# Kernel optimization log

Measured on AMD Instinct MI355X. Metric: run time of the kernel, lower is better.

## Reference

```python
import jax, jax.numpy as jnp
import numpy as np

N_HEAD = 16
NEG = -1e9

def setup_inputs() -> dict:
    key = jax.random.key(0)
    ks = jax.random.split(key, 11)
    B, T, D = 2, 2048, 1024
    s = 0.02
    return {
        "x": jax.random.normal(ks[0], (B, T, D), jnp.float32),
        "mask": jax.random.randint(ks[1], (B, T), 0, 2).astype(bool),
        "wq": jax.random.normal(ks[2], (D, D), jnp.float32) * s,
        "bq": jax.random.normal(ks[3], (D,), jnp.float32) * s,
        "wk": jax.random.normal(ks[4], (D, D), jnp.float32) * s,
        "bk": jax.random.normal(ks[5], (D,), jnp.float32) * s,
        "wv": jax.random.normal(ks[6], (D, D), jnp.float32) * s,
        "bv": jax.random.normal(ks[7], (D,), jnp.float32) * s,
        "wp": jax.random.normal(ks[8], (D, D), jnp.float32) * s,
        "bp": jax.random.normal(ks[9], (D,), jnp.float32) * s,
    }

def reference(x, mask, wq, bq, wk, bk, wv, bv, wp, bp):
    B, T, V = x.shape
    H = N_HEAD
    hd = V // H
    # project and split heads: [B, H, T, hd]
    def heads(w, b):
        return (x @ w + b).reshape(B, T, H, hd).transpose(0, 2, 1, 3)
    q = heads(wq, bq)
    k = heads(wk, bk)
    v = heads(wv, bv)
    # scores [B, H, T, T]
    att = jnp.einsum("bhqd,bhkd->bhqk", q, k) * (1.0 / jnp.sqrt(jnp.float32(hd)))
    # key-padding mask: True -> masked. broadcast [B,1,1,T] == torch's [B,1,T,T]
    att = jnp.where(mask[:, None, None, :], NEG, att)
    att = jax.nn.softmax(att, axis=-1)
    out = jnp.einsum("bhqk,bhkd->bhqd", att, v)  # [B,H,T,hd]
    out = out.transpose(0, 2, 1, 3).reshape(B, T, V)
    out = out @ wp + bp
    # dropout is identity in eval mode
    return out, att
```

## Files before the change

kernel.cpp:

```cpp
#include <hip/hip_runtime.h>
#include <stdint.h>
#include <stddef.h>


typedef __attribute__((ext_vector_type(8))) short short8;
typedef __attribute__((ext_vector_type(4))) float f32x4;

#define LDS_AS __attribute__((address_space(3)))
#define GLB_AS __attribute__((address_space(1)))

static __device__ __forceinline__ unsigned short f2bf(float f) {
  union { float f; uint32_t u; } v; v.f = f;
  uint32_t u = v.u;
  return (unsigned short)((u + 0x7fffu + ((u >> 16) & 1u)) >> 16);
}

static __device__ __forceinline__ void gload16(const void* g, void* l) {
  __builtin_amdgcn_global_load_lds((const GLB_AS uint32_t*)g, (LDS_AS uint32_t*)l, 16, 0, 0);
}

static __device__ __forceinline__ f32x4 mfma16(short8 a, short8 b, f32x4 c) {
  return __builtin_amdgcn_mfma_f32_16x16x32_bf16(a, b, c, 0, 0, 0);
}

__global__ void k_convert_x(const float* __restrict__ x, unsigned short* __restrict__ xb) {
  int i = blockIdx.x * 256 + threadIdx.x;
  float4 v = ((const float4*)x)[i];
  ushort4 o;
  o.x = f2bf(v.x); o.y = f2bf(v.y); o.z = f2bf(v.z); o.w = f2bf(v.w);
  ((ushort4*)xb)[i] = o;
}

__global__ void k_mask(const int* __restrict__ m, float* __restrict__ madd) {
  int i = blockIdx.x * 256 + threadIdx.x;
  madd[i] = m[i] ? -1e9f : 0.0f;
}

__global__ void k_transpose_w(const float* __restrict__ w0, const float* __restrict__ w1,
                              const float* __restrict__ w2, const float* __restrict__ w3,
                              unsigned short* __restrict__ o0, unsigned short* __restrict__ o1,
                              unsigned short* __restrict__ o2, unsigned short* __restrict__ o3) {
  int bx = blockIdx.x;
  int which = bx >> 8, tile = bx & 255;
  const float* w = which == 0 ? w0 : which == 1 ? w1 : which == 2 ? w2 : w3;
  unsigned short* o = which == 0 ? o0 : which == 1 ? o1 : which == 2 ? o2 : o3;
  int k0 = (tile >> 4) << 6, n0 = (tile & 15) << 6;
  __shared__ float t[64][65];
  int tid = threadIdx.x;
  int r = tid >> 4, c4 = (tid & 15) << 2;
#pragma unroll
  for (int i = 0; i < 4; i++) {
    int row = r + (i << 4);
    float4 v = *(const float4*)(w + (size_t)(k0 + row) * 1024 + n0 + c4);
    t[row][c4] = v.x; t[row][c4 + 1] = v.y; t[row][c4 + 2] = v.z; t[row][c4 + 3] = v.w;
  }
  __syncthreads();
#pragma unroll
  for (int i = 0; i < 4; i++) {
    int n = r + (i << 4);
    ushort4 ov;
    ov.x = f2bf(t[c4 + 0][n]); ov.y = f2bf(t[c4 + 1][n]);
    ov.z = f2bf(t[c4 + 2][n]); ov.w = f2bf(t[c4 + 3][n]);
    *(ushort4*)(o + (size_t)(n0 + n) * 1024 + k0 + c4) = ov;
  }
}

static __device__ __forceinline__ void gemm_tile(const unsigned short* __restrict__ A,
                                                 const unsigned short* __restrict__ Bt,
                                                 int m0, int n0,
                                                 f32x4 acc[4][4], char* ldsA, char* ldsB) {
  const int tid = threadIdx.x;
  const int l = tid & 63;
  const int wr = tid >> 7;
  const int wc = (tid >> 6) & 1;
  const int arow0 = wr * 64 + (l & 15);
  const int brow0 = wc * 64 + (l & 15);
  const int srow = tid >> 3;
  const int sgi = tid & 7;

  for (int kt = 0; kt < 1024; kt += 64) {
    __syncthreads();
#pragma unroll
    for (int c = 0; c < 4; c++) {
      int row = c * 32 + srow;
      int soff = (sgi ^ (row & 7)) << 3;
      gload16(A + (size_t)(m0 + row) * 1024 + kt + soff, ldsA + (c * 256 + tid) * 16);
      gload16(Bt + (size_t)(n0 + row) * 1024 + kt + soff, ldsB + (c * 256 + tid) * 16);
    }
    asm volatile("s_waitcnt vmcnt(0)" ::: "memory");
    __syncthreads();
#pragma unroll
    for (int ks = 0; ks < 2; ks++) {
      const int kbyte = ks * 64 + ((l >> 4) << 4);
      short8 a[4], b[4];
#pragma unroll
      for (int i = 0; i < 4; i++) {
        int row = arow0 + i * 16;
        a[i] = *(const short8*)(ldsA + row * 128 + (kbyte ^ ((row & 7) << 4)));
      }
#pragma unroll
      for (int j = 0; j < 4; j++) {
        int row = brow0 + j * 16;
        b[j] = *(const short8*)(ldsB + row * 128 + (kbyte ^ ((row & 7) << 4)));
      }
#pragma unroll
      for (int i = 0; i < 4; i++)
#pragma unroll
        for (int j = 0; j < 4; j++)
          acc[i][j] = mfma16(a[i], b[j], acc[i][j]);
    }
  }
}

__global__ __launch_bounds__(256) void k_gemm_qkv(const unsigned short* __restrict__ xb,
    const unsigned short* __restrict__ wqt, const unsigned short* __restrict__ wkt,
    const unsigned short* __restrict__ wvt,
    const float* __restrict__ bq, const float* __restrict__ bk, const float* __restrict__ bv,
    unsigned short* __restrict__ Q, unsigned short* __restrict__ K, unsigned short* __restrict__ Vt) {
  __shared__ __align__(16) char smem[32768];
  char* ldsA = smem;
  char* ldsB = smem + 16384;
  const int mat = blockIdx.y >> 3;
  const int nb = blockIdx.y & 7;
  const unsigned short* Bt = mat == 0 ? wqt : mat == 1 ? wkt : wvt;
  const float* bias = mat == 0 ? bq : mat == 1 ? bk : bv;
  const int m0 = blockIdx.x * 128, n0 = nb * 128;

  f32x4 acc[4][4] = {};
  gemm_tile(xb, Bt, m0, n0, acc, ldsA, ldsB);

  const int tid = threadIdx.x, l = tid & 63;
  const int wr = tid >> 7, wc = (tid >> 6) & 1;
  if (mat < 2) {
    unsigned short* O = (mat == 0) ? Q : K;
#pragma unroll
    for (int j = 0; j < 4; j++) {
      int col = n0 + wc * 64 + j * 16 + (l & 15);
      float bv_ = bias[col];
      int h = col >> 6, d = col & 63;
#pragma unroll
      for (int i = 0; i < 4; i++) {
        int row0 = m0 + wr * 64 + i * 16 + ((l >> 4) << 2);
#pragma unroll
        for (int e = 0; e < 4; e++) {
          int row = row0 + e;
          int b = row >> 11, t = row & 2047;
          O[(((size_t)(b * 16 + h)) * 2048 + t) * 64 + d] = f2bf(acc[i][j][e] + bv_);
        }
      }
    }
  } else {
#pragma unroll
    for (int j = 0; j < 4; j++) {
      int col = n0 + wc * 64 + j * 16 + (l & 15);
      float bv_ = bias[col];
      int h = col >> 6, d = col & 63;
#pragma unroll
      for (int i = 0; i < 4; i++) {
        int row0 = m0 + wr * 64 + i * 16 + ((l >> 4) << 2);
        int b = row0 >> 11, t0 = row0 & 2047;
        ushort4 pk;
        pk.x = f2bf(acc[i][j][0] + bv_);
        pk.y = f2bf(acc[i][j][1] + bv_);
        pk.z = f2bf(acc[i][j][2] + bv_);
        pk.w = f2bf(acc[i][j][3] + bv_);
        *(ushort4*)(Vt + ((size_t)(b * 16 + h) * 64 + d) * 2048 + t0) = pk;
      }
    }
  }
}

__global__ __launch_bounds__(256) void k_gemm_proj(const unsigned short* __restrict__ ctx,
    const unsigned short* __restrict__ wpt, const float* __restrict__ bp,
    float* __restrict__ out) {
  __shared__ __align__(16) char smem[32768];
  char* ldsA = smem;
  char* ldsB = smem + 16384;
  const int m0 = blockIdx.x * 128, n0 = blockIdx.y * 128;
  f32x4 acc[4][4] = {};
  gemm_tile(ctx, wpt, m0, n0, acc, ldsA, ldsB);
  const int tid = threadIdx.x, l = tid & 63;
  const int wr = tid >> 7, wc = (tid >> 6) & 1;
#pragma unroll
  for (int j = 0; j < 4; j++) {
    int col = n0 + wc * 64 + j * 16 + (l & 15);
    float bv_ = bp[col];
#pragma unroll
    for (int i = 0; i < 4; i++) {
      int row0 = m0 + wr * 64 + i * 16 + ((l >> 4) << 2);
#pragma unroll
      for (int e = 0; e < 4; e++)
        out[(size_t)(row0 + e) * 1024 + col] = acc[i][j][e] + bv_;
    }
  }
}

__global__ __launch_bounds__(256) void k_attn(const unsigned short* __restrict__ Q,
    const unsigned short* __restrict__ K, const unsigned short* __restrict__ Vt,
    const float* __restrict__ maskadd, float* __restrict__ att,
    unsigned short* __restrict__ ctx) {
  __shared__ __align__(16) char smem[57344];
  char* Ql = smem;
  char* Kl = smem + 8192;
  char* Vl = smem + 24576;
  char* Pl = smem + 40960;

  const int bid = (blockIdx.x & 7) * 128 + (blockIdx.x >> 3);
  const int qb = bid & 31, bh = bid >> 5;
  const int b = bh >> 4, h = bh & 15;
  const int tid = threadIdx.x, w = tid >> 6, l = tid & 63;
  const int qbase = qb * 64;

  const unsigned short* Qg = Q + (size_t)bh * 2048 * 64;
  const unsigned short* Kg = K + (size_t)bh * 2048 * 64;
  const unsigned short* Vg = Vt + (size_t)bh * 64 * 2048;
  const float* mg = maskadd + b * 2048;
  const float scale = 0.125f;

#pragma unroll
  for (int c = 0; c < 2; c++) {
    int g = c * 256 + tid;
    int row = g >> 3, gi = tid & 7;
    gload16(Qg + (size_t)(qbase + row) * 64 + ((gi ^ (row & 7)) << 3), Ql + g * 16);
  }
  asm volatile("s_waitcnt vmcnt(0)" ::: "memory");
  __syncthreads();

  short8 qf[2];
  {
    int row = w * 16 + (l & 15);
#pragma unroll
    for (int ks = 0; ks < 2; ks++) {
      int kbyte = ks * 64 + ((l >> 4) << 4);
      qf[ks] = *(const short8*)(Ql + row * 128 + (kbyte ^ ((row & 7) << 4)));
    }
  }

  float mrow[4], srow[4];
#pragma unroll
  for (int e = 0; e < 4; e++) { mrow[e] = -1e30f; srow[e] = 0.0f; }

  for (int ch = 0; ch < 16; ch++) {
    __syncthreads();
#pragma unroll
    for (int c = 0; c < 4; c++) {
      int g = c * 256 + tid;
      int row = g >> 3, gi = tid & 7;
      gload16(Kg + (size_t)(ch * 128 + row) * 64 + ((gi ^ (row & 7)) << 3), Kl + g * 16);
    }
    asm volatile("s_waitcnt vmcnt(0)" ::: "memory");
    __syncthreads();

    float lv[8][4];
    float cmax[4] = {-1e30f, -1e30f, -1e30f, -1e30f};
#pragma unroll
    for (int nt = 0; nt < 8; nt++) {
      f32x4 s = {};
#pragma unroll
      for (int ks = 0; ks < 2; ks++) {
        int row = nt * 16 + (l & 15);
        int kbyte = ks * 64 + ((l >> 4) << 4);
        short8 kf = *(const short8*)(Kl + row * 128 + (kbyte ^ ((row & 7) << 4)));
        s = mfma16(qf[ks], kf, s);
      }
      int key = ch * 128 + nt * 16 + (l & 15);
      float madd = mg[key];
#pragma unroll
      for (int e = 0; e < 4; e++) {
        lv[nt][e] = s[e] * scale + madd;
        cmax[e] = fmaxf(cmax[e], lv[nt][e]);
      }
    }
#pragma unroll
    for (int e = 0; e < 4; e++) {
      float cs = 0.0f;
#pragma unroll
      for (int nt = 0; nt < 8; nt++) cs += __expf(lv[nt][e] - cmax[e]);
      float mn = fmaxf(mrow[e], cmax[e]);
      srow[e] = srow[e] * __expf(mrow[e] - mn) + cs * __expf(cmax[e] - mn);
      mrow[e] = mn;
    }
  }

  float invs[4];
#pragma unroll
  for (int e = 0; e < 4; e++) {
    float m = mrow[e], s = srow[e];
#pragma unroll
    for (int msk = 1; msk < 16; msk <<= 1) {
      float mo = __shfl_xor(m, msk);
      float so = __shfl_xor(s, msk);
      float mn = fmaxf(m, mo);
      s = s * __expf(m - mn) + so * __expf(mo - mn);
      m = mn;
    }
    mrow[e] = m;
    invs[e] = 1.0f / s;
  }

  f32x4 o[4] = {};
  for (int ch = 0; ch < 16; ch++) {
    __syncthreads();
#pragma unroll
    for (int c = 0; c < 4; c++) {
      int g = c * 256 + tid;
      int row = g >> 3, gi = tid & 7;
      gload16(Kg + (size_t)(ch * 128 + row) * 64 + ((gi ^ (row & 7)) << 3), Kl + g * 16);
    }
#pragma unroll
    for (int c = 0; c < 4; c++) {
      int g = c * 256 + tid;
      int d = g >> 4, gi = tid & 15;
      gload16(Vg + (size_t)d * 2048 + ch * 128 + ((gi ^ (d & 7)) << 3), Vl + g * 16);
    }
    asm volatile("s_waitcnt vmcnt(0)" ::: "memory");
    __syncthreads();

#pragma unroll
    for (int nt = 0; nt < 8; nt++) {
      f32x4 s = {};
#pragma unroll
      for (int ks = 0; ks < 2; ks++) {
        int row = nt * 16 + (l & 15);
        int kbyte = ks * 64 + ((l >> 4) << 4);
        short8 kf = *(const short8*)(Kl + row * 128 + (kbyte ^ ((row & 7) << 4)));
        s = mfma16(qf[ks], kf, s);
      }
      int key = ch * 128 + nt * 16 + (l & 15);
      float madd = mg[key];
#pragma unroll
      for (int e = 0; e < 4; e++) {
        float p = __expf(s[e] * scale + madd - mrow[e]) * invs[e];
        int qrow = qbase + w * 16 + ((l >> 4) << 2) + e;
        __builtin_nontemporal_store(p, att + ((size_t)bh * 2048 + qrow) * 2048 + key);
        int pr = w * 16 + ((l >> 4) << 2) + e;
        int cb = (nt * 16 + (l & 15)) * 2;
        *(unsigned short*)(Pl + pr * 256 + (cb ^ ((pr & 7) << 4))) = f2bf(p);
      }
    }
#pragma unroll
    for (int ks = 0; ks < 4; ks++) {
      int prow = w * 16 + (l & 15);
      int kb = ks * 64 + ((l >> 4) << 4);
      short8 pa = *(const short8*)(Pl + prow * 256 + (kb ^ ((prow & 7) << 4)));
#pragma unroll
      for (int dt = 0; dt < 4; dt++) {
        int vrow = dt * 16 + (l & 15);
        short8 vb = *(const short8*)(Vl + vrow * 256 + (kb ^ ((vrow & 7) << 4)));
        o[dt] = mfma16(pa, vb, o[dt]);
      }
    }
  }

#pragma unroll
  for (int dt = 0; dt < 4; dt++) {
#pragma unroll
    for (int e = 0; e < 4; e++) {
      int t = qbase + w * 16 + ((l >> 4) << 2) + e;
      int col = h * 64 + dt * 16 + (l & 15);
      ctx[((size_t)(b * 2048 + t)) * 1024 + col] = f2bf(o[dt][e]);
    }
  }
}

extern "C" void kernel_launch(void* const* d_in, const int* in_sizes, int n_in,
                              void* d_out, int out_size, void* d_ws, size_t ws_size,
                              hipStream_t stream) {
  const float* x  = (const float*)d_in[0];
  const int* mask = (const int*)d_in[1];
  const float* wq = (const float*)d_in[2];
  const float* bq = (const float*)d_in[3];
  const float* wk = (const float*)d_in[4];
  const float* bk = (const float*)d_in[5];
  const float* wv = (const float*)d_in[6];
  const float* bv = (const float*)d_in[7];
  const float* wp = (const float*)d_in[8];
  const float* bp = (const float*)d_in[9];

  float* out = (float*)d_out;
  float* att = out + 4194304;

  char* ws = (char*)d_ws;
  unsigned short* xb  = (unsigned short*)(ws);
  unsigned short* wqt = (unsigned short*)(ws + 8388608);
  unsigned short* wkt = (unsigned short*)(ws + 10485760);
  unsigned short* wvt = (unsigned short*)(ws + 12582912);
  unsigned short* wpt = (unsigned short*)(ws + 14680064);
  unsigned short* Qw  = (unsigned short*)(ws + 16777216);
  unsigned short* Kw  = (unsigned short*)(ws + 25165824);
  unsigned short* Vtw = (unsigned short*)(ws + 33554432);
  unsigned short* ctx = (unsigned short*)(ws + 41943040);
  float* madd         = (float*)(ws + 50331648);

  k_convert_x<<<4096, 256, 0, stream>>>(x, xb);
  k_mask<<<16, 256, 0, stream>>>(mask, madd);
  k_transpose_w<<<1024, 256, 0, stream>>>(wq, wk, wv, wp, wqt, wkt, wvt, wpt);
  k_gemm_qkv<<<dim3(32, 24), 256, 0, stream>>>(xb, wqt, wkt, wvt, bq, bk, bv, Qw, Kw, Vtw);
  k_attn<<<1024, 256, 0, stream>>>(Qw, Kw, Vtw, madd, att, ctx);
  k_gemm_proj<<<dim3(32, 8), 256, 0, stream>>>(ctx, wpt, bp, out);
}
```

Baseline: 266.3 us.

## Process 128 query rows per attention block to halve K/V reloads

Each attention block now handles 128 query rows instead of 64. Each wave owns two 16-row sub-tiles, so every K and V tile loaded into LDS is reused across twice as many queries, and the grid shrinks from 1024 to 512 blocks. The P buffer is aliased onto the Q staging area, with an extra barrier after Q fragments are read, and LDS grows to 64KB. The trade-off is higher register pressure, fewer blocks per CU and fewer total blocks, which may reduce occupancy and latency hiding. The kernel is likely bound by the fp32 attention-matrix write, so the K/V savings may matter little.

```diff
diff --git a/kernel.cpp b/kernel.cpp
--- a/kernel.cpp
+++ b/kernel.cpp
@@ -199,17 +199,17 @@
     const unsigned short* __restrict__ K, const unsigned short* __restrict__ Vt,
     const float* __restrict__ maskadd, float* __restrict__ att,
     unsigned short* __restrict__ ctx) {
-  __shared__ __align__(16) char smem[57344];
+  __shared__ __align__(16) char smem[65536];
+  char* Pl = smem;
   char* Ql = smem;
-  char* Kl = smem + 8192;
-  char* Vl = smem + 24576;
-  char* Pl = smem + 40960;
-
-  const int bid = (blockIdx.x & 7) * 128 + (blockIdx.x >> 3);
-  const int qb = bid & 31, bh = bid >> 5;
+  char* Kl = smem + 32768;
+  char* Vl = smem + 49152;
+
+  const int bid = (blockIdx.x & 7) * 64 + (blockIdx.x >> 3);
+  const int qb = bid & 15, bh = bid >> 4;
   const int b = bh >> 4, h = bh & 15;
   const int tid = threadIdx.x, w = tid >> 6, l = tid & 63;
-  const int qbase = qb * 64;
+  const int qbase = qb * 128;
 
   const unsigned short* Qg = Q + (size_t)bh * 2048 * 64;
   const unsigned short* Kg = K + (size_t)bh * 2048 * 64;
@@ -218,7 +218,7 @@
   const float scale = 0.125f;
 
 #pragma unroll
-  for (int c = 0; c < 2; c++) {
+  for (int c = 0; c < 4; c++) {
     int g = c * 256 + tid;
     int row = g >> 3, gi = tid & 7;
     gload16(Qg + (size_t)(qbase + row) * 64 + ((gi ^ (row & 7)) << 3), Ql + g * 16);
@@ -226,19 +226,23 @@
   asm volatile("s_waitcnt vmcnt(0)" ::: "memory");
   __syncthreads();
 
-  short8 qf[2];
-  {
-    int row = w * 16 + (l & 15);
+  short8 qf[2][2];
+#pragma unroll
+  for (int m = 0; m < 2; m++) {
+    int row = w * 32 + m * 16 + (l & 15);
 #pragma unroll
     for (int ks = 0; ks < 2; ks++) {
       int kbyte = ks * 64 + ((l >> 4) << 4);
-      qf[ks] = *(const short8*)(Ql + row * 128 + (kbyte ^ ((row & 7) << 4)));
-    }
-  }
-
-  float mrow[4], srow[4];
-#pragma unroll
-  for (int e = 0; e < 4; e++) { mrow[e] = -1e30f; srow[e] = 0.0f; }
+      qf[m][ks] = *(const short8*)(Ql + row * 128 + (kbyte ^ ((row & 7) << 4)));
+    }
+  }
+  __syncthreads();
+
+  float mrow[2][4], srow[2][4];
+#pragma unroll
+  for (int m = 0; m < 2; m++)
+#pragma unroll
+    for (int e = 0; e < 4; e++) { mrow[m][e] = -1e30f; srow[m][e] = 0.0f; }
 
   for (int ch = 0; ch < 16; ch++) {
     __syncthreads();
@@ -251,54 +255,59 @@
     asm volatile("s_waitcnt vmcnt(0)" ::: "memory");
     __syncthreads();
 
-    float lv[8][4];
-    float cmax[4] = {-1e30f, -1e30f, -1e30f, -1e30f};
-#pragma unroll
-    for (int nt = 0; nt < 8; nt++) {
-      f32x4 s = {};
-#pragma unroll
-      for (int ks = 0; ks < 2; ks++) {
-        int row = nt * 16 + (l & 15);
-        int kbyte = ks * 64 + ((l >> 4) << 4);
-        short8 kf = *(const short8*)(Kl + row * 128 + (kbyte ^ ((row & 7) << 4)));
-        s = mfma16(qf[ks], kf, s);
-      }
-      int key = ch * 128 + nt * 16 + (l & 15);
-      float madd = mg[key];
+#pragma unroll
+    for (int m = 0; m < 2; m++) {
+      float lv[8][4];
+      float cmax[4] = {-1e30f, -1e30f, -1e30f, -1e30f};
+#pragma unroll
+      for (int nt = 0; nt < 8; nt++) {
+        f32x4 s = {};
+#pragma unroll
+        for (int ks = 0; ks < 2; ks++) {
+          int row = nt * 16 + (l & 15);
+          int kbyte = ks * 64 + ((l >> 4) << 4);
+          short8 kf = *(const short8*)(Kl + row * 128 + (kbyte ^ ((row & 7) << 4)));
+          s = mfma16(qf[m][ks], kf, s);
+        }
+        int key = ch * 128 + nt * 16 + (l & 15);
+        float madd = mg[key];
+#pragma unroll
+        for (int e = 0; e < 4; e++) {
+          lv[nt][e] = s[e] * scale + madd;
+          cmax[e] = fmaxf(cmax[e], lv[nt][e]);
+        }
+      }
 #pragma unroll
       for (int e = 0; e < 4; e++) {
-        lv[nt][e] = s[e] * scale + madd;
-        cmax[e] = fmaxf(cmax[e], lv[nt][e]);
-      }
-    }
+        float cs = 0.0f;
+#pragma unroll
+        for (int nt = 0; nt < 8; nt++) cs += __expf(lv[nt][e] - cmax[e]);
+        float mn = fmaxf(mrow[m][e], cmax[e]);
+        srow[m][e] = srow[m][e] * __expf(mrow[m][e] - mn) + cs * __expf(cmax[e] - mn);
+        mrow[m][e] = mn;
+      }
+    }
+  }
+
+  float invs[2][4];
+#pragma unroll
+  for (int m = 0; m < 2; m++)
 #pragma unroll
     for (int e = 0; e < 4; e++) {
-      float cs = 0.0f;
-#pragma unroll
-      for (int nt = 0; nt < 8; nt++) cs += __expf(lv[nt][e] - cmax[e]);
-      float mn = fmaxf(mrow[e], cmax[e]);
-      srow[e] = srow[e] * __expf(mrow[e] - mn) + cs * __expf(cmax[e] - mn);
-      mrow[e] = mn;
-    }
-  }
-
-  float invs[4];
-#pragma unroll
-  for (int e = 0; e < 4; e++) {
-    float m = mrow[e], s = srow[e];
-#pragma unroll
-    for (int msk = 1; msk < 16; msk <<= 1) {
-      float mo = __shfl_xor(m, msk);
-      float so = __shfl_xor(s, msk);
-      float mn = fmaxf(m, mo);
-      s = s * __expf(m - mn) + so * __expf(mo - mn);
-      m = mn;
-    }
-    mrow[e] = m;
-    invs[e] = 1.0f / s;
-  }
-
-  f32x4 o[4] = {};
+      float mm = mrow[m][e], s = srow[m][e];
+#pragma unroll
+      for (int msk = 1; msk < 16; msk <<= 1) {
+        float mo = __shfl_xor(mm, msk);
+        float so = __shfl_xor(s, msk);
+        float mn = fmaxf(mm, mo);
+        s = s * __expf(mm - mn) + so * __expf(mo - mn);
+        mm = mn;
+      }
+      mrow[m][e] = mm;
+      invs[m][e] = 1.0f / s;
+    }
+
+  f32x4 o[2][4] = {};
   for (int ch = 0; ch < 16; ch++) {
     __syncthreads();
 #pragma unroll
@@ -317,50 +326,55 @@
     __syncthreads();
 
 #pragma unroll
-    for (int nt = 0; nt < 8; nt++) {
-      f32x4 s = {};
-#pragma unroll
-      for (int ks = 0; ks < 2; ks++) {
-        int row = nt * 16 + (l & 15);
-        int kbyte = ks * 64 + ((l >> 4) << 4);
-        short8 kf = *(const short8*)(Kl + row * 128 + (kbyte ^ ((row & 7) << 4)));
-        s = mfma16(qf[ks], kf, s);
-      }
-      int key = ch * 128 + nt * 16 + (l & 15);
-      float madd = mg[key];
+    for (int m = 0; m < 2; m++) {
+#pragma unroll
+      for (int nt = 0; nt < 8; nt++) {
+        f32x4 s = {};
+#pragma unroll
+        for (int ks = 0; ks < 2; ks++) {
+          int row = nt * 16 + (l & 15);
+          int kbyte = ks * 64 + ((l >> 4) << 4);
+          short8 kf = *(const short8*)(Kl + row * 128 + (kbyte ^ ((row & 7) << 4)));
+          s = mfma16(qf[m][ks], kf, s);
+        }
+        int key = ch * 128 + nt * 16 + (l & 15);
+        float madd = mg[key];
+#pragma unroll
+        for (int e = 0; e < 4; e++) {
+          float p = __expf(s[e] * scale + madd - mrow[m][e]) * invs[m][e];
+          int qrow = qbase + w * 32 + m * 16 + ((l >> 4) << 2) + e;
+          __builtin_nontemporal_store(p, att + ((size_t)bh * 2048 + qrow) * 2048 + key);
+          int pr = w * 32 + m * 16 + ((l >> 4) << 2) + e;
+          int cb = (nt * 16 + (l & 15)) * 2;
+          *(unsigned short*)(Pl + pr * 256 + (cb ^ ((pr & 7) << 4))) = f2bf(p);
+        }
+      }
+#pragma unroll
+      for (int ks = 0; ks < 4; ks++) {
+        int prow = w * 32 + m * 16 + (l & 15);
+        int kb = ks * 64 + ((l >> 4) << 4);
+        short8 pa = *(const short8*)(Pl + prow * 256 + (kb ^ ((prow & 7) << 4)));
+#pragma unroll
+        for (int dt = 0; dt < 4; dt++) {
+          int vrow = dt * 16 + (l & 15);
+          short8 vb = *(const short8*)(Vl + vrow * 256 + (kb ^ ((vrow & 7) << 4)));
+          o[m][dt] = mfma16(pa, vb, o[m][dt]);
+        }
+      }
+    }
+  }
+
+#pragma unroll
+  for (int m = 0; m < 2; m++)
+#pragma unroll
+    for (int dt = 0; dt < 4; dt++) {
 #pragma unroll
       for (int e = 0; e < 4; e++) {
-        float p = __expf(s[e] * scale + madd - mrow[e]) * invs[e];
-        int qrow = qbase + w * 16 + ((l >> 4) << 2) + e;
-        __builtin_nontemporal_store(p, att + ((size_t)bh * 2048 + qrow) * 2048 + key);
-        int pr = w * 16 + ((l >> 4) << 2) + e;
-        int cb = (nt * 16 + (l & 15)) * 2;
-        *(unsigned short*)(Pl + pr * 256 + (cb ^ ((pr & 7) << 4))) = f2bf(p);
-      }
-    }
-#pragma unroll
-    for (int ks = 0; ks < 4; ks++) {
-      int prow = w * 16 + (l & 15);
-      int kb = ks * 64 + ((l >> 4) << 4);
-      short8 pa = *(const short8*)(Pl + prow * 256 + (kb ^ ((prow & 7) << 4)));
-#pragma unroll
-      for (int dt = 0; dt < 4; dt++) {
-        int vrow = dt * 16 + (l & 15);
-        short8 vb = *(const short8*)(Vl + vrow * 256 + (kb ^ ((vrow & 7) << 4)));
-        o[dt] = mfma16(pa, vb, o[dt]);
-      }
-    }
-  }
-
-#pragma unroll
-  for (int dt = 0; dt < 4; dt++) {
-#pragma unroll
-    for (int e = 0; e < 4; e++) {
-      int t = qbase + w * 16 + ((l >> 4) << 2) + e;
-      int col = h * 64 + dt * 16 + (l & 15);
-      ctx[((size_t)(b * 2048 + t)) * 1024 + col] = f2bf(o[dt][e]);
-    }
-  }
+        int t = qbase + w * 32 + m * 16 + ((l >> 4) << 2) + e;
+        int col = h * 64 + dt * 16 + (l & 15);
+        ctx[((size_t)(b * 2048 + t)) * 1024 + col] = f2bf(o[m][dt][e]);
+      }
+    }
 }
 
 extern "C" void kernel_launch(void* const* d_in, const int* in_sizes, int n_in,
@@ -396,6 +410,6 @@
   k_mask<<<16, 256, 0, stream>>>(mask, madd);
   k_transpose_w<<<1024, 256, 0, stream>>>(wq, wk, wv, wp, wqt, wkt, wvt, wpt);
   k_gemm_qkv<<<dim3(32, 24), 256, 0, stream>>>(xb, wqt, wkt, wvt, bq, bk, bv, Qw, Kw, Vtw);
-  k_attn<<<1024, 256, 0, stream>>>(Qw, Kw, Vtw, madd, att, ctx);
+  k_attn<<<512, 256, 0, stream>>>(Qw, Kw, Vtw, madd, att, ctx);
   k_gemm_proj<<<dim3(32, 8), 256, 0, stream>>>(ctx, wpt, bp, out);
 }
```

Result: slower. 305.6 us (+14.8%).

## Transpose score MFMA so each lane owns one query row with vectorized stores

Applied to the files above, without the earlier changes.

Swaps the MFMA operand order for QK^T so each lane holds four consecutive keys of a single query row instead of four query rows. The row max and sum can then be tracked as one scalar per lane, the mask is read as a float4, the attention probabilities are written as 16-byte nontemporal stores, and the bf16 P tile is written to LDS as 8-byte packs. This targets the scattered 4-byte global stores of the large attention matrix and cuts per-row softmax bookkeeping. The cross-lane reduction now spans lanes 16 to 48 apart instead of within 16 lanes.

```diff
diff --git a/kernel.cpp b/kernel.cpp
--- a/kernel.cpp
+++ b/kernel.cpp
@@ -209,6 +209,8 @@
   const int qb = bid & 31, bh = bid >> 5;
   const int b = bh >> 4, h = bh & 15;
   const int tid = threadIdx.x, w = tid >> 6, l = tid & 63;
+  const int hi = l >> 4;
+  const int qr = l & 15;
   const int qbase = qb * 64;
 
   const unsigned short* Qg = Q + (size_t)bh * 2048 * 64;
@@ -228,18 +230,15 @@
 
   short8 qf[2];
   {
-    int row = w * 16 + (l & 15);
+    int row = w * 16 + qr;
 #pragma unroll
     for (int ks = 0; ks < 2; ks++) {
-      int kbyte = ks * 64 + ((l >> 4) << 4);
+      int kbyte = ks * 64 + (hi << 4);
       qf[ks] = *(const short8*)(Ql + row * 128 + (kbyte ^ ((row & 7) << 4)));
     }
   }
 
-  float mrow[4], srow[4];
-#pragma unroll
-  for (int e = 0; e < 4; e++) { mrow[e] = -1e30f; srow[e] = 0.0f; }
-
+  float m_run = -1e30f, s_run = 0.0f;
   for (int ch = 0; ch < 16; ch++) {
     __syncthreads();
 #pragma unroll
@@ -252,53 +251,48 @@
     __syncthreads();
 
     float lv[8][4];
-    float cmax[4] = {-1e30f, -1e30f, -1e30f, -1e30f};
+    float cmax = -1e30f;
 #pragma unroll
     for (int nt = 0; nt < 8; nt++) {
       f32x4 s = {};
 #pragma unroll
       for (int ks = 0; ks < 2; ks++) {
-        int row = nt * 16 + (l & 15);
-        int kbyte = ks * 64 + ((l >> 4) << 4);
+        int row = nt * 16 + qr;
+        int kbyte = ks * 64 + (hi << 4);
         short8 kf = *(const short8*)(Kl + row * 128 + (kbyte ^ ((row & 7) << 4)));
-        s = mfma16(qf[ks], kf, s);
-      }
-      int key = ch * 128 + nt * 16 + (l & 15);
-      float madd = mg[key];
-#pragma unroll
-      for (int e = 0; e < 4; e++) {
-        lv[nt][e] = s[e] * scale + madd;
-        cmax[e] = fmaxf(cmax[e], lv[nt][e]);
-      }
-    }
-#pragma unroll
-    for (int e = 0; e < 4; e++) {
-      float cs = 0.0f;
-#pragma unroll
-      for (int nt = 0; nt < 8; nt++) cs += __expf(lv[nt][e] - cmax[e]);
-      float mn = fmaxf(mrow[e], cmax[e]);
-      srow[e] = srow[e] * __expf(mrow[e] - mn) + cs * __expf(cmax[e] - mn);
-      mrow[e] = mn;
-    }
-  }
-
-  float invs[4];
-#pragma unroll
-  for (int e = 0; e < 4; e++) {
-    float m = mrow[e], s = srow[e];
-#pragma unroll
-    for (int msk = 1; msk < 16; msk <<= 1) {
-      float mo = __shfl_xor(m, msk);
-      float so = __shfl_xor(s, msk);
-      float mn = fmaxf(m, mo);
-      s = s * __expf(m - mn) + so * __expf(mo - mn);
-      m = mn;
-    }
-    mrow[e] = m;
-    invs[e] = 1.0f / s;
-  }
+        s = mfma16(kf, qf[ks], s);
+      }
+      float4 m4 = *(const float4*)(mg + ch * 128 + nt * 16 + (hi << 2));
+      lv[nt][0] = s[0] * scale + m4.x;
+      lv[nt][1] = s[1] * scale + m4.y;
+      lv[nt][2] = s[2] * scale + m4.z;
+      lv[nt][3] = s[3] * scale + m4.w;
+#pragma unroll
+      for (int e = 0; e < 4; e++) cmax = fmaxf(cmax, lv[nt][e]);
+    }
+    float cs = 0.0f;
+#pragma unroll
+    for (int nt = 0; nt < 8; nt++)
+#pragma unroll
+      for (int e = 0; e < 4; e++) cs += __expf(lv[nt][e] - cmax);
+    float mn = fmaxf(m_run, cmax);
+    s_run = s_run * __expf(m_run - mn) + cs * __expf(cmax - mn);
+    m_run = mn;
+  }
+
+#pragma unroll
+  for (int msk = 16; msk < 64; msk <<= 1) {
+    float mo = __shfl_xor(m_run, msk);
+    float so = __shfl_xor(s_run, msk);
+    float mn = fmaxf(m_run, mo);
+    s_run = s_run * __expf(m_run - mn) + so * __expf(mo - mn);
+    m_run = mn;
+  }
+  const float mfin = m_run;
+  const float invs = 1.0f / s_run;
 
   f32x4 o[4] = {};
+  const size_t arow = ((size_t)bh * 2048 + qbase + w * 16 + qr) * 2048;
   for (int ch = 0; ch < 16; ch++) {
     __syncthreads();
 #pragma unroll
@@ -321,31 +315,34 @@
       f32x4 s = {};
 #pragma unroll
       for (int ks = 0; ks < 2; ks++) {
-        int row = nt * 16 + (l & 15);
-        int kbyte = ks * 64 + ((l >> 4) << 4);
+        int row = nt * 16 + qr;
+        int kbyte = ks * 64 + (hi << 4);
         short8 kf = *(const short8*)(Kl + row * 128 + (kbyte ^ ((row & 7) << 4)));
-        s = mfma16(qf[ks], kf, s);
-      }
-      int key = ch * 128 + nt * 16 + (l & 15);
-      float madd = mg[key];
-#pragma unroll
-      for (int e = 0; e < 4; e++) {
-        float p = __expf(s[e] * scale + madd - mrow[e]) * invs[e];
-        int qrow = qbase + w * 16 + ((l >> 4) << 2) + e;
-        __builtin_nontemporal_store(p, att + ((size_t)bh * 2048 + qrow) * 2048 + key);
-        int pr = w * 16 + ((l >> 4) << 2) + e;
-        int cb = (nt * 16 + (l & 15)) * 2;
-        *(unsigned short*)(Pl + pr * 256 + (cb ^ ((pr & 7) << 4))) = f2bf(p);
-      }
+        s = mfma16(kf, qf[ks], s);
+      }
+      float4 m4 = *(const float4*)(mg + ch * 128 + nt * 16 + (hi << 2));
+      f32x4 p;
+      p[0] = __expf(s[0] * scale + m4.x - mfin) * invs;
+      p[1] = __expf(s[1] * scale + m4.y - mfin) * invs;
+      p[2] = __expf(s[2] * scale + m4.z - mfin) * invs;
+      p[3] = __expf(s[3] * scale + m4.w - mfin) * invs;
+      __builtin_nontemporal_store(
+          p, (f32x4*)(att + arow + ch * 128 + nt * 16 + (hi << 2)));
+      uint32_t plo = (uint32_t)f2bf(p[0]) | ((uint32_t)f2bf(p[1]) << 16);
+      uint32_t phi = (uint32_t)f2bf(p[2]) | ((uint32_t)f2bf(p[3]) << 16);
+      int prow = w * 16 + qr;
+      int cb = (nt * 16 + (hi << 2)) * 2;
+      uint2 pk; pk.x = plo; pk.y = phi;
+      *(uint2*)(Pl + prow * 256 + (cb ^ ((prow & 7) << 4))) = pk;
     }
 #pragma unroll
     for (int ks = 0; ks < 4; ks++) {
-      int prow = w * 16 + (l & 15);
-      int kb = ks * 64 + ((l >> 4) << 4);
+      int prow = w * 16 + qr;
+      int kb = ks * 64 + (hi << 4);
       short8 pa = *(const short8*)(Pl + prow * 256 + (kb ^ ((prow & 7) << 4)));
 #pragma unroll
       for (int dt = 0; dt < 4; dt++) {
-        int vrow = dt * 16 + (l & 15);
+        int vrow = dt * 16 + qr;
         short8 vb = *(const short8*)(Vl + vrow * 256 + (kb ^ ((vrow & 7) << 4)));
         o[dt] = mfma16(pa, vb, o[dt]);
       }
@@ -356,8 +353,8 @@
   for (int dt = 0; dt < 4; dt++) {
 #pragma unroll
     for (int e = 0; e < 4; e++) {
-      int t = qbase + w * 16 + ((l >> 4) << 2) + e;
-      int col = h * 64 + dt * 16 + (l & 15);
+      int t = qbase + w * 16 + (hi << 2) + e;
+      int col = h * 64 + dt * 16 + qr;
       ctx[((size_t)(b * 2048 + t)) * 1024 + col] = f2bf(o[dt][e]);
     }
   }
```

New measurement: 316.7 us. 18.9% more time.
